# Kernel tuning notes

Hardware: AMD Instinct MI355X
Metric: run time of the kernel (lower is better)

## Reference

```python
import math
import numpy as np
import jax, jax.numpy as jnp

LMAX1, LMAX2, LMAX3 = 20, 10, 5
B_IN, RES1, RES2, RES3 = 60, 20, 10, 6
BATCH = 8


def _fact(n):
    return math.factorial(n)


def wigner_d(l, betas):
    # small Wigner-d, complex-m ordering m=-l..l; betas: [N] -> [N, 2l+1, 2l+1]
    betas = np.asarray(betas, dtype=np.float64)
    cb, sb = np.cos(betas / 2.0), np.sin(betas / 2.0)
    d = np.zeros(betas.shape + (2 * l + 1, 2 * l + 1))
    for i, mp in enumerate(range(-l, l + 1)):
        for j, m in enumerate(range(-l, l + 1)):
            pref = math.sqrt(_fact(l + mp) * _fact(l - mp) * _fact(l + m) * _fact(l - m))
            val = np.zeros_like(betas)
            for k in range(max(0, m - mp), min(l + m, l - mp) + 1):
                den = _fact(l + m - k) * _fact(k) * _fact(mp - m + k) * _fact(l - mp - k)
                val = val + ((-1.0) ** (mp - m + k)) * (pref / den) * cb ** (2 * l + m - mp - 2 * k) * sb ** (mp - m + 2 * k)
            d[..., i, j] = val
    return d


def real_U(l):
    # complex SH -> real SH change of basis
    U = np.zeros((2 * l + 1, 2 * l + 1), dtype=np.complex128)
    U[l, l] = 1.0
    for m in range(1, l + 1):
        s = (-1.0) ** m
        U[l + m, l - m] = 1.0 / math.sqrt(2.0)
        U[l + m, l + m] = s / math.sqrt(2.0)
        U[l - m, l - m] = 1j / math.sqrt(2.0)
        U[l - m, l + m] = -1j * s / math.sqrt(2.0)
    return U


def wigner_d_real(l, betas):
    U = real_U(l)
    d = wigner_d(l, betas).astype(np.complex128)
    return np.einsum('ai,nij,bj->nab', U, d, U.conj()).real


def _trig(ang, l):
    m = np.arange(-l, l + 1)
    return np.cos(np.outer(ang, m)), np.sin(np.outer(ang, m))


def flat_wigner_points(lmax, a, b, g):
    # real Wigner D on arbitrary points via D = Z(alpha) d_real(beta) Z(gamma)
    blocks = []
    for l in range(lmax + 1):
        dr = wigner_d_real(l, b)  # [N,M,M]
        cA, sA = _trig(a, l)
        cG, sG = _trig(g, l)
        T = cG[:, None, :] * dr - sG[:, None, :] * dr[:, :, ::-1]
        D = cA[:, :, None] * T + sA[:, :, None] * T[:, ::-1, :]
        blocks.append(math.sqrt(2 * l + 1) * D.reshape(len(a), -1))
    return np.concatenate(blocks, -1).astype(np.float32)


def flat_wigner_grid(lmax, alphas, betas, gammas):
    # product-grid version, flatten order (alpha, beta, gamma)
    na, nb, ng = len(alphas), len(betas), len(gammas)
    blocks = []
    for l in range(lmax + 1):
        dr = wigner_d_real(l, betas)  # [nb,M,M]
        cA, sA = _trig(alphas, l)
        cG, sG = _trig(gammas, l)
        T = cG[None, :, None, :] * dr[:, None] - sG[None, :, None, :] * dr[:, None, :, ::-1]  # [nb,ng,M,M]
        D = cA[:, None, None, :, None] * T[None] + sA[:, None, None, :, None] * T[None, :, :, ::-1, :]
        blocks.append(math.sqrt(2 * l + 1) * D.reshape(na * nb * ng, -1))
    return np.concatenate(blocks, -1).astype(np.float32)


def sph_points(lmax, a, b):
    # component-normalized real SH: Y_l(alpha,beta) = sqrt(2l+1) D^l(alpha,beta,0)[:,m=0]
    cols = []
    for l in range(lmax + 1):
        dr = wigner_d_real(l, b)[:, :, l]
        cA, sA = _trig(a, l)
        cols.append(math.sqrt(2 * l + 1) * (cA * dr + sA * dr[:, ::-1]))
    return np.concatenate(cols, -1).astype(np.float32)


def sph_grid_cols(lmax, alphas, betas):
    cols = []
    for l in range(lmax + 1):
        dr = wigner_d_real(l, betas)[:, :, l]  # [nb,M]
        cA, sA = _trig(alphas, l)
        Y = cA[None] * dr[:, None] + sA[None] * dr[:, None, ::-1]  # [nb,na,M]
        cols.append(math.sqrt(2 * l + 1) * Y)
    return np.concatenate(cols, -1)


def so3_grid(n):
    a = np.arange(n) / n * 2 * math.pi
    b = (np.arange(n) + 0.5) / n * math.pi
    g = np.arange(n) / n * 2 * math.pi
    return a, b, g


def so3_transforms(lmax_in, lmax_out, n):
    a, b, g = so3_grid(n)
    D_in = flat_wigner_grid(lmax_in, a, b, g)
    D_out = flat_wigner_grid(lmax_out, a, b, g)
    qw = np.tile(np.sin(b)[None, :, None], (n, 1, n)).ravel() * math.pi / (2.0 * n ** 3)
    return jnp.asarray(D_in), jnp.asarray((qw[:, None] * D_out).astype(np.float32))


def s2_near_identity_grid(max_beta=math.pi / 8, n_alpha=8, n_beta=3):
    beta = np.arange(1, n_beta + 1) * max_beta / n_beta
    alpha = np.linspace(0, 2 * math.pi, n_alpha + 1)[:-1]
    A, B = np.meshgrid(alpha, beta, indexing='ij')
    return A.ravel(), B.ravel()


def so3_near_identity_grid(max_beta=math.pi / 8, max_gamma=2 * math.pi, n_alpha=8, n_beta=3, n_gamma=8):
    beta = np.arange(1, n_beta + 1) * max_beta / n_beta
    alpha = np.linspace(0, 2 * math.pi, n_alpha)[:-1]
    pre_gamma = np.linspace(-max_gamma, max_gamma, n_gamma)
    A, B, preC = np.meshgrid(alpha, beta, pre_gamma, indexing='ij')
    return A.ravel(), B.ravel(), (preC - A).ravel()


# ---- constant buffers (built once with numpy, like e3nn register_buffer) ----
_betas = (np.arange(B_IN) + 0.5) / B_IN * math.pi
_alphas = np.arange(B_IN) / B_IN * 2 * math.pi
_Y = sph_grid_cols(LMAX1, _alphas, _betas)  # [nb,na,441]
_qw = np.sin(_betas) * math.pi / (2.0 * B_IN * B_IN)
FROM_S2 = jnp.asarray((_Y * _qw[:, None, None]).reshape(B_IN * B_IN, -1).astype(np.float32))  # [3600,441]

_a2, _b2 = s2_near_identity_grid()
Y_K = jnp.asarray(sph_points(LMAX1, _a2, _b2))  # [24,441]
_a3, _b3, _g3 = so3_near_identity_grid()
D_K2 = jnp.asarray(flat_wigner_points(LMAX2, _a3, _b3, _g3))  # [168,1771]
D_K3 = jnp.asarray(flat_wigner_points(LMAX3, _a3, _b3, _g3))  # [168,286]

D1_IN, D1_BWD = so3_transforms(LMAX1, LMAX2, RES1)  # [8000,12341], [8000,1771]
D2_IN, D2_BWD = so3_transforms(LMAX2, LMAX3, RES2)  # [1000,1771],  [1000,286]
D3_IN, D3_BWD = so3_transforms(LMAX3, 0, RES3)      # [216,286],    [216,1]


def _s2_linear(x, psi, lmax):
    # x [B,f_in,(lmax+1)^2] (mult-1 per l) -> so3 irreps [B,f_out,sum(2l+1)^2]
    B, fi = x.shape[0], x.shape[1]
    outs = []
    for l in range(lmax + 1):
        s, e = l * l, (l + 1) * (l + 1)
        ol = jnp.einsum('bim,iou->boum', x[:, :, s:e], psi[:, :, s:e]) / math.sqrt(fi)
        outs.append(ol.reshape(B, ol.shape[1], -1))
    return jnp.concatenate(outs, axis=-1)


def _so3_linear(x, psi, lmax):
    # block per-l linear: mult (2l+1) -> mult (2l+1)
    B, fi = x.shape[0], x.shape[1]
    outs, off = [], 0
    for l in range(lmax + 1):
        d = 2 * l + 1
        xl = x[:, :, off:off + d * d].reshape(B, fi, d, d)
        pl = psi[:, :, off:off + d * d].reshape(fi, -1, d, d)
        ol = jnp.einsum('bium,iouv->bovm', xl, pl) / math.sqrt(fi * d)
        outs.append(ol.reshape(B, ol.shape[1], -1))
        off += d * d
    return jnp.concatenate(outs, axis=-1)


def _so3_act(x, D_in, D_bwd):
    # SO3Activation: to SO(3) grid, relu, back to (lower) band-limited coeffs
    f = jax.nn.relu(jnp.einsum('bfi,ni->bfn', x, D_in))
    return jnp.einsum('bfn,ni->bfi', f, D_bwd)


def _forward(x, conv1_w, conv2_w, conv3_w, fc_w1, fc_b1, fc_w2, fc_b2):
    B = x.shape[0]
    xg = jnp.swapaxes(x, -1, -2).reshape(B, -1)  # (beta, alpha) grid, flattened
    coeff = (xg @ FROM_S2)[:, None, :]           # FromS2Grid -> [B,1,441]
    psi1 = jnp.einsum('ni,xyn->xyi', Y_K, conv1_w) / math.sqrt(Y_K.shape[0])
    h = _s2_linear(coeff, psi1, LMAX1)           # [B,64,12341]
    h = _so3_act(h, D1_IN, D1_BWD)               # [B,64,1771]
    psi2 = jnp.einsum('ni,xyn->xyi', D_K2, conv2_w) / math.sqrt(D_K2.shape[0])
    h = _so3_linear(h, psi2, LMAX2)              # [B,128,1771]
    h = _so3_act(h, D2_IN, D2_BWD)               # [B,128,286]
    psi3 = jnp.einsum('ni,xyn->xyi', D_K3, conv3_w) / math.sqrt(D_K3.shape[0])
    h = _so3_linear(h, psi3, LMAX3)              # [B,256,286]
    h = _so3_act(h, D3_IN, D3_BWD)[:, :, 0]      # lmax_out=0 -> [B,256]
    h = jax.nn.relu(h @ fc_w1 + fc_b1)           # dropout is identity in eval
    return h @ fc_w2 + fc_b2


def setup_inputs() -> dict:
    key = jax.random.key(0)
    ks = jax.random.split(key, 6)
    return {
        'x': jax.random.normal(ks[0], (BATCH, B_IN, B_IN), dtype=jnp.float32),
        'conv1_w': jax.random.normal(ks[1], (1, 64, 24), dtype=jnp.float32),
        'conv2_w': jax.random.normal(ks[2], (64, 128, 168), dtype=jnp.float32),
        'conv3_w': jax.random.normal(ks[3], (128, 256, 168), dtype=jnp.float32),
        'fc_w1': jax.random.normal(ks[4], (256, 128), dtype=jnp.float32) / math.sqrt(256.0),
        'fc_b1': jnp.zeros((128,), jnp.float32),
        'fc_w2': jax.random.normal(ks[5], (128, 10), dtype=jnp.float32) / math.sqrt(128.0),
        'fc_b2': jnp.zeros((10,), jnp.float32),
    }


def reference(x, conv1_w, conv2_w, conv3_w, fc_w1, fc_b1, fc_w2, fc_b2):
    return _forward(x, conv1_w, conv2_w, conv3_w, fc_w1, fc_b1, fc_w2, fc_b2)
```

## Files before the change

### kernel.cpp

```cpp
#include <hip/hip_runtime.h>

#define PI_D 3.14159265358979323846

constexpr int S_L20 = 12341;
constexpr int S_L10 = 1771;
constexpr int S_L5  = 286;
constexpr int C_L20 = 441;

typedef float f4 __attribute__((ext_vector_type(4)));
typedef float f2 __attribute__((ext_vector_type(2)));
template<int W> struct VW;
template<> struct VW<4> { using T = f4; };
template<> struct VW<2> { using T = f2; };

__host__ __device__ __forceinline__ int loff(int l) { return l*(4*l*l-1)/3; }

__device__ __forceinline__ int isqrt_dev(int c) {
  int l = (int)sqrtf((float)c);
  while ((l+1)*(l+1) <= c) ++l;
  while (l*l > c) --l;
  return l;
}

__device__ double d_small(int l, int mp, int m, const double* cpw, const double* spw, const double* fact) {
// ... 48 lines not shown
                                                float* t3c, float* t3s,
                                                unsigned* lut10, unsigned* lut5) {
  __shared__ double cpw[44], spw[44], fact[44];
  int b = blockIdx.x;
  int tid = threadIdx.x;
  if (b < 846) {
    float* out; int lmax, S, mode, gridn, p, chunk;
    if (b < 260)      { out=dr20g1; lmax=20; S=S_L20; mode=0; gridn=20; p=b/13;        chunk=b%13; }
    else if (b < 596) { int i=b-260; out=drK2;   lmax=10; S=S_L10; mode=1; gridn=0;  p=i/2; chunk=i%2; }
    else if (b < 636) { int i=b-596; out=dr10g1; lmax=10; S=S_L10; mode=0; gridn=20; p=i/2; chunk=i%2; }
    else if (b < 656) { int i=b-636; out=dr10g2; lmax=10; S=S_L10; mode=0; gridn=10; p=i/2; chunk=i%2; }
    else if (b < 824) { int i=b-656; out=drK3;   lmax=5;  S=S_L5;  mode=1; gridn=0;  p=i;   chunk=0; }
    else if (b < 834) { int i=b-824; out=dr5g2;  lmax=5;  S=S_L5;  mode=0; gridn=10; p=i;   chunk=0; }
    else if (b < 840) { int i=b-834; out=dr5g3;  lmax=5;  S=S_L5;  mode=0; gridn=6;  p=i;   chunk=0; }
    else              { int i=b-840; out=dr0g3;  lmax=0;  S=1;     mode=0; gridn=6;  p=i;   chunk=0; }
    double beta_ = beta_of(mode, p, gridn);
    if (tid == 0) {
      double cb_ = cos(beta_*0.5), sb_ = sin(beta_*0.5);
      cpw[0]=1.0; spw[0]=1.0; fact[0]=1.0;
      for (int i_=1;i_<44;++i_){cpw[i_]=cpw[i_-1]*cb_; spw[i_]=spw[i_-1]*sb_; fact[i_]=fact[i_-1]*(double)i_;}
    }
    __syncthreads();
    int base = chunk*1024;
    int end = min(S, base + 1024);
    for (int t = base + tid; t < end; t += 256) {
      int l = 0; while (l < lmax && t >= loff(l+1)) ++l;
      int j = t - loff(l), d = 2*l+1;
      int a = j/d, bb = j%d;
      double v = dr_elem(l, a-l, bb-l, cpw, spw, fact) * sqrt(2.0*l+1.0);
      out[(size_t)p*S + t] = (float)v;
    }
  } else if (b < 930) {
    int bb = b - 846;
    float* out; int mode, gridn, p;
    if (bb < 60) { out = drc60; mode = 0; gridn = 60; p = bb; }
    else         { out = drc24; mode = 2; gridn = 0;  p = bb - 60; }
    double beta_ = beta_of(mode, p, gridn);
    if (tid == 0) {
      double cb_ = cos(beta_*0.5), sb_ = sin(beta_*0.5);
      cpw[0]=1.0; spw[0]=1.0; fact[0]=1.0;
      for (int i_=1;i_<44;++i_){cpw[i_]=cpw[i_-1]*cb_; spw[i_]=spw[i_-1]*sb_; fact[i_]=fact[i_-1]*(double)i_;}
    }
    __syncthreads();
    for (int t = tid; t < C_L20; t += 256) {
      int l = isqrt_dev(t);
      int u = t - l*l - l;
      double v;
      if (u < 0) v = 0.0;
      else if (u == 0) v = d_small(l,0,0,cpw,spw,fact);
      else {
        double sp = (u&1)? -1.0: 1.0;
        v = 0.70710678118654752440*(d_small(l,-u,0,cpw,spw,fact) + sp*d_small(l,u,0,cpw,spw,fact));
      }
      out[(size_t)p*C_L20 + t] = (float)(v * sqrt(2.0*l+1.0));
    }
  } else if (b < 933) {
    int t = (b - 930)*256 + tid;
    if (t < 420) {
      int k = t/20, ig = t%20;
      double ang = (double)k*(double)ig*(2.0*PI_D/20.0);
      t1c[t] = (float)cos(ang); t1s[t] = (float)sin(ang);
    } else if (t < 530) {
      int i = t-420, k = i/10, ig = i%10;
      double ang = (double)k*(double)ig*(2.0*PI_D/10.0);
      t2c[i] = (float)cos(ang); t2s[i] = (float)sin(ang);
    } else if (t < 566) {
      int i = t-530, k = i/6, ig = i%6;
      double ang = (double)k*(double)ig*(2.0*PI_D/6.0);
      t3c[i] = (float)cos(ang); t3s[i] = (float)sin(ang);
    }
  } else {
    int t = (b - 933)*256 + tid;
    unsigned* lut; int s, lmax;
    if (t < S_L10) { lut = lut10; s = t; lmax = 10; }
    else if (t < S_L10 + S_L5) { lut = lut5; s = t - S_L10; lmax = 5; }
    else return;
    int l = 0; while (l < lmax && s >= loff(l+1)) ++l;
    int j = s - loff(l), d = 2*l+1;
    int u = j/d, v = j - u*d;
    lut[s] = (unsigned)l | ((unsigned)u<<8) | ((unsigned)v<<16);
  }
}

__global__ __launch_bounds__(256) void k_tab2(const float* __restrict__ drc60, float* __restrict__ FS2T,
                                              const float* __restrict__ drc24, const float* __restrict__ w1,
                                              float* __restrict__ psi1,
                                              const float* __restrict__ drk2, float* __restrict__ DK2,
                                              const float* __restrict__ drk3, float* __restrict__ DK3) {
  int b = blockIdx.x, tid = threadIdx.x;
  if (b < 6202) {
    int e = b*256 + tid;
    if (e >= 441*3600) return;
    int c = e / 3600, k = e % 3600;
    int ia = k / 60, ib = k % 60;
    int l = isqrt_dev(c);
    int u = c - l*l - l;
    double alpha = (double)ia*(2.0*PI_D/60.0);
    double beta  = ((double)ib + 0.5)*(PI_D/60.0);
    double drp = (double)drc60[ib*441 + c];
    double drn = (double)drc60[ib*441 + (c - 2*u)];
    double val = cos((double)u*alpha)*drp + sin((double)u*alpha)*drn;
    FS2T[e] = (float)(val * (sin(beta)*PI_D/(2.0*60.0*60.0)));
  } else if (b < 6313) {
    int e = (b - 6202)*256 + tid;
    if (e >= 64*441) return;
    int o = e / 441, c = e % 441;
    int l = isqrt_dev(c);
    int u = c - l*l - l;
    float acc = 0.f;
    for (int p = 0; p < 24; ++p) {
      double alpha = (double)(p/3)*(PI_D/4.0);
      double y = cos((double)u*alpha)*(double)drc24[p*441+c] + sin((double)u*alpha)*(double)drc24[p*441 + (c-2*u)];
      acc += (float)y * w1[o*24 + p];
    }
    psi1[e] = acc * 0.20412414523193150818f;
  } else {
    int e0 = (b - 6313)*256 + tid;
    const float* drk; float* DK; int S, NP, lmax, e;
    if (e0 < 168*1772) { drk = drk2; DK = DK2; S = S_L10; NP = 1772; lmax = 10; e = e0; }
    else { e = e0 - 168*1772; if (e >= 168*288) return; drk = drk3; DK = DK3; S = S_L5; NP = 288; lmax = 5; }
    int n = e / NP, idx = e % NP;
    if (idx >= S) { DK[e] = 0.f; return; }
    int l = 0; while (l < lmax && idx >= loff(l+1)) ++l;
    int j = idx - loff(l), d = 2*l+1;
    int iu = j/d, im = j%d;
    int u = iu - l, m = im - l;
    int i3 = n/24, k3 = n%8;
    double alpha = (double)i3*(2.0*PI_D/7.0);
    double gamma = (-2.0*PI_D + (double)k3*(4.0*PI_D/7.0)) - alpha;
    const float* drb = drk + (size_t)n*S + loff(l);
    double d_um   = drb[iu*d+im];
    double d_umn  = drb[iu*d + (d-1-im)];
    double d_unm  = drb[(d-1-iu)*d + im];
    double d_unmn = drb[(d-1-iu)*d + (d-1-im)];
    double cA = cos((double)u*alpha), sA = sin((double)u*alpha);
    double cG = cos((double)m*gamma), sG = sin((double)m*gamma);
    DK[e] = (float)(cA*(cG*d_um - sG*d_umn) + sA*(cG*d_unm - sG*d_unmn));
  }
}

__device__ __forceinline__ void gemm_body(const float* __restrict__ A, const float* __restrict__ B,
                                          const unsigned* __restrict__ lut, float* __restrict__ C,
                                          int M, int N, int NP, int K, int FO, int tm, int tn, float alpha,
                                          float (*As)[16][68], float (*Bs)[16][68], int tid) {
  int ty = tid/16, tx = tid%16;
  int arr = tid>>2, akq = (tid&3)*4;
  int bkk = tid>>4, bcq = (tid&15)*4;
  const float* Arow = A + (size_t)(tm + arr)*K;
  const f4 FZ = 0.f;
  float acc[4][4] = {};
  f4 ra, rb;
#define LOADC(k0)                                                        \
  if ((k0) + 16 <= K) {                                                  \
    ra = *(const f4*)&Arow[(k0) + akq];                                  \
    rb = *(const f4*)&B[(size_t)((k0) + bkk)*NP + tn + bcq];             \
  } else {                                                               \
    _Pragma("unroll")                                                    \
    for (int jj = 0; jj < 4; ++jj) {                                     \
      int k = (k0) + akq + jj;                                           \
      ra[jj] = (k < K) ? Arow[k] : 0.f;                                  \
    }                                                                    \
    int k2 = (k0) + bkk;                                                 \
    rb = (k2 < K) ? *(const f4*)&B[(size_t)k2*NP + tn + bcq] : FZ;       \
  }
#define STOREC(b)                                                        \
  {                                                                      \
    _Pragma("unroll")                                                    \
    for (int jj = 0; jj < 4; ++jj) As[b][akq+jj][arr] = ra[jj];          \
    *(f4*)&Bs[b][bkk][bcq] = rb;                                         \
  }
  LOADC(0);
  STOREC(0);
  __syncthreads();
  int cur = 0;
  for (int k0 = 0; k0 < K; k0 += 16) {
    bool nxt = (k0 + 16) < K;
    if (nxt) { LOADC(k0 + 16); }
#pragma unroll
    for (int kk = 0; kk < 16; ++kk) {
      f4 av = *(const f4*)&As[cur][kk][ty*4];
      f4 bv = *(const f4*)&Bs[cur][kk][tx*4];
#pragma unroll
      for (int q = 0; q < 4; ++q)
#pragma unroll
        for (int r2 = 0; r2 < 4; ++r2) acc[q][r2] += av[q]*bv[r2];
    }
    if (nxt) { STOREC(cur ^ 1); __syncthreads(); cur ^= 1; }
  }
#undef LOADC
#undef STOREC
  for (int q = 0; q < 4; ++q) {
    int r = tm + ty*4 + q; if (r >= M) continue;
    int i = r / FO, o = r - i*FO;
    for (int r2 = 0; r2 < 4; ++r2) {
      int c = tn + tx*4 + r2; if (c >= N) continue;
      unsigned e = lut[c];
      int l = e & 255, u = (e>>8)&255, v = (e>>16)&255;
      int d = 2*l+1;
      C[(size_t)M*loff(l) + (size_t)(i*d+u)*(FO*d) + o*d + v] = alpha*acc[q][r2];
    }
  }
}

__global__ __launch_bounds__(256) void k_gemmc(const float* __restrict__ A1, const float* __restrict__ B1,
                                               const unsigned* __restrict__ lut1, float* __restrict__ C1,
                                               int M1, int N1, int NP1, int FO1,
                                               const float* __restrict__ A2, const float* __restrict__ B2,
                                               const unsigned* __restrict__ lut2, float* __restrict__ C2,
                                               int M2, int N2, int NP2, int FO2,
                                               int K, int nbx1, int nb1, int nbx2, int nb12, float alpha,
                                               const float* __restrict__ x, const float* __restrict__ fs2T,
                                               float* __restrict__ coeff) {
  __shared__ __align__(16) float As[2][16][68], Bs[2][16][68];
  int bid = blockIdx.x, tid = threadIdx.x;
  if (bid < nb1) {
    int tm = (bid % nbx1)*64, tn = (bid / nbx1)*64;
    gemm_body(A1, B1, lut1, C1, M1, N1, NP1, K, FO1, tm, tn, alpha, As, Bs, tid);
  } else if (bid < nb12) {
    bid -= nb1;
    int tm = (bid % nbx2)*64, tn = (bid / nbx2)*64;
    gemm_body(A2, B2, lut2, C2, M2, N2, NP2, K, FO2, tm, tn, alpha, As, Bs, tid);
  } else {
    int c = bid - nb12;
    float acc[8] = {};
    const float* fr = fs2T + (size_t)c*3600;
    for (int k = tid; k < 3600; k += 256) {
      float w = fr[k];
#pragma unroll
      for (int b = 0; b < 8; ++b) acc[b] += w * x[b*3600 + k];
    }
    float* red = (float*)As;
#pragma unroll
    for (int b = 0; b < 8; ++b) red[b*256 + tid] = acc[b];
    __syncthreads();
    for (int s = 128; s > 0; s >>= 1) {
      if (tid < s) {
#pragma unroll
        for (int b = 0; b < 8; ++b) red[b*256 + tid] += red[b*256 + tid + s];
      }
      __syncthreads();
    }
    if (tid < 8) coeff[tid*441 + c] = red[tid*256];
  }
}

__global__ __launch_bounds__(256) void k_anapack(const float* __restrict__ part, const unsigned* __restrict__ lut,
                                                 float* __restrict__ hA, int FI, int S, int nch) {
  int e = blockIdx.x*256 + threadIdx.x;
  int total = 8*FI*S;
  if (e >= total) return;
  int bi = e / S, s = e - bi*S;
  float a = 0.f;
  for (int c = 0; c < nch; ++c) a += part[(size_t)c*total + e];
  unsigned u3 = lut[s];
  int l = u3 & 255, u = (u3>>8)&255, m = (u3>>16)&255;
  int d = 2*l+1;
  int b = bi / FI, i = bi - b*FI;
  hA[(size_t)8*FI*loff(l) + (size_t)(b*d+m)*(FI*d) + i*d + u] = a;
}

__global__ __launch_bounds__(256) void k_linsk(const float* __restrict__ hA, const float* __restrict__ psiP,
                                               float* __restrict__ part, int FI, int FO, int S,
                                               int maxNT, int KC) {
  int l = blockIdx.z;
  int d = 2*l+1, off = loff(l);
  int Ml = 8*d, Nl = FO*d, Kl = FI*d;
  int tm = blockIdx.x*64;
  int tn = ((int)blockIdx.y % maxNT)*64;
  int kci = (int)blockIdx.y / maxNT;
  int k0s = kci*KC;
  if (tm >= Ml || tn >= Nl || k0s >= Kl) return;
  int k1s = min(Kl, k0s + KC);
  float alpha = 1.0f/sqrtf((float)(FI*d));
  const float* Ab = hA + (size_t)8*FI*off;
  const float* Bb = psiP + (size_t)FI*FO*off;
  __shared__ __align__(16) float As[2][16][68], Bs[2][16][68];
  int tid = threadIdx.x, ty = tid/16, tx = tid%16;
  int arr = tid>>2, akq = (tid&3)*4;
  int bkk = tid>>4, bcq = (tid&15)*4;
  bool aok = (tm + arr) < Ml;
  const float* Arow = Ab + (size_t)(tm + arr)*Kl;
  const f4 FZ = 0.f;
  float acc[4][4] = {};
  f4 ra, rb;
#define LOADL(k0)                                                        \
  {                                                                      \
    ra = aok ? *(const f4*)&Arow[(k0) + akq] : FZ;                       \
    rb = *(const f4*)&Bb[(size_t)((k0) + bkk)*Nl + tn + bcq];            \
  }
#define STOREL(b)                                                        \
  {                                                                      \
    _Pragma("unroll")                                                    \
    for (int jj = 0; jj < 4; ++jj) As[b][akq+jj][arr] = ra[jj];          \
    *(f4*)&Bs[b][bkk][bcq] = rb;                                         \
  }
  LOADL(k0s);
  STOREL(0);
  __syncthreads();
  int cur = 0;
  for (int k0 = k0s; k0 < k1s; k0 += 16) {
    bool nxt = (k0 + 16) < k1s;
    if (nxt) { LOADL(k0 + 16); }
#pragma unroll
    for (int kk = 0; kk < 16; ++kk) {
      f4 av = *(const f4*)&As[cur][kk][ty*4];
      f4 bv = *(const f4*)&Bs[cur][kk][tx*4];
#pragma unroll
      for (int q = 0; q < 4; ++q)
#pragma unroll
        for (int r2 = 0; r2 < 4; ++r2) acc[q][r2] += av[q]*bv[r2];
    }
    if (nxt) { STOREL(cur ^ 1); __syncthreads(); cur ^= 1; }
  }
#undef LOADL
#undef STOREL
  size_t pbase = (size_t)kci * (size_t)8*FO*S;
  for (int q = 0; q < 4; ++q) {
    int r = tm + ty*4 + q; if (r >= Ml) continue;
    int b = r / d, m = r - b*d;
    for (int r2 = 0; r2 < 4; ++r2) {
      int c = tn + tx*4 + r2; if (c >= Nl) continue;
      int o = c / d, v = c - o*d;
      part[pbase + (size_t)(b*FO + o)*S + off + v*d + m] = alpha*acc[q][r2];
    }
  }
}

template<int L, int NG, int F, int BS>
__global__ __launch_bounds__(BS) void k_syn1b(const float* __restrict__ psi1, const float* __restrict__ coeff,
                                              const float* __restrict__ drg,
                                              const float* __restrict__ gtck, const float* __restrict__ gtsk,
                                              float* __restrict__ fw) {
  constexpr int LH = L+1;
  constexpr int LH2 = LH*LH;
  constexpr int S = (L+1)*(2*L+1)*(2*L+3)/3;
  constexpr int IGB = 4;
  constexpr int NGB = NG / IGB;
  __shared__ float PF[4*LH2], Q1F[4*LH2], Q2F[4*LH2], Q3F[4*LH2];
  __shared__ __align__(16) float uni[4*C_L20];
  __shared__ __align__(16) float tck[LH*NG], tsk[LH*NG];
  float* psi_s  = uni;
  float* coef_s = uni + 2*C_L20;
  float* Rc = uni;
  float* Rs = uni + LH*NG;
  int ib = blockIdx.x, f0 = blockIdx.y*2, b0 = blockIdx.z*2;
  int tid = threadIdx.x;
  for (int t = tid; t < C_L20; t += BS) {
    psi_s[t]          = psi1[f0*C_L20 + t];
    psi_s[C_L20 + t]  = psi1[(f0+1)*C_L20 + t];
    coef_s[t]         = coeff[b0*C_L20 + t];
    coef_s[C_L20 + t] = coeff[(b0+1)*C_L20 + t];
  }
  for (int t = tid; t < LH*NG; t += BS) { tck[t] = gtck[t]; tsk[t] = gtsk[t]; }
  __syncthreads();
  const float* drb = drg + (size_t)ib*S;
  for (int t = tid; t < LH2; t += BS) {
    int i = t / LH, j = t % LH;
    int lmin = max(i, j);
    float P[4] = {}, Q1[4] = {}, Q2[4] = {}, Q3[4] = {};
    int d = 2*lmin+1;
    int j2 = 2*j;
    int drip = loff(lmin) + (lmin+i)*d + (lmin-j);
    int drim = loff(lmin) + (lmin-i)*d + (lmin-j);
    int hA = lmin*lmin + lmin + i;
    int hB = lmin*lmin + lmin - i;
    int hM = lmin*lmin + lmin - j;
    int hMp = lmin*lmin + lmin + j;
    for (int l = lmin; l <= L; ++l) {
      float ap_ = drb[drip], app = drb[drip + j2];
      float am_ = 0.f, amp = 0.f;
      if (i > 0) { am_ = drb[drim]; amp = drb[drim + j2]; }
      float eP[2], oP[2], eM[2], oM[2];
#pragma unroll
      for (int cb = 0; cb < 2; ++cb) {
        float hm = coef_s[cb*C_L20 + hM], hmn = coef_s[cb*C_L20 + hMp];
        eP[cb] = ap_*hm + app*hmn;  oP[cb] = app*hm - ap_*hmn;
        eM[cb] = am_*hm + amp*hmn;  oM[cb] = amp*hm - am_*hmn;
      }
#pragma unroll
      for (int cf = 0; cf < 2; ++cf) {
        float ha = psi_s[cf*C_L20 + hA], hb = psi_s[cf*C_L20 + hB];
#pragma unroll
        for (int cb = 0; cb < 2; ++cb) {
          int cs = cb*2 + cf;
          P[cs]  += ha*eP[cb] + hb*eM[cb];
          Q1[cs] += ha*oP[cb] + hb*oM[cb];
          Q2[cs] += hb*eP[cb] - ha*eM[cb];
          Q3[cs] += hb*oP[cb] - ha*oM[cb];
        }
      }
      drip += d*d + d + 2*(l+i) + 3;
      drim += d*d + d + 2*(l-i) + 3;
      int hstep = d + 1;
      hA += hstep; hB += hstep; hM += hstep; hMp += hstep;
      d += 2;
    }
    if (j == 0) {
#pragma unroll
      for (int cs = 0; cs < 4; ++cs) { P[cs] *= 0.5f; Q2[cs] *= 0.5f; }
    }
#pragma unroll
    for (int cs = 0; cs < 4; ++cs) {
      PF[cs*LH2 + t] = P[cs]; Q1F[cs*LH2 + t] = Q1[cs];
      Q2F[cs*LH2 + t] = Q2[cs]; Q3F[cs*LH2 + t] = Q3[cs];
    }
  }
  __syncthreads();
  double beta = ((double)ib + 0.5) * (PI_D / (double)NG);
  float qwv = (float)(sin(beta) * PI_D / (2.0*(double)NG*(double)NG*(double)NG));
  for (int cs = 0; cs < 4; ++cs) {
    int cf = cs & 1, cb = cs >> 1;
    for (int t = tid; t < LH*NGB; t += BS) {
      int i = t / NGB, ig0 = (t % NGB)*IGB;
      f4 rc = 0.f, rs = 0.f;
      const float* Pr  = PF  + cs*LH2 + i*LH;
      const float* Q1r = Q1F + cs*LH2 + i*LH;
      const float* Q2r = Q2F + cs*LH2 + i*LH;
      const float* Q3r = Q3F + cs*LH2 + i*LH;
      for (int k = 0; k <= L; ++k) {
        float p = Pr[k], q1 = Q1r[k], q2 = Q2r[k], q3 = Q3r[k];
        f4 c = *(const f4*)(tck + k*NG + ig0);
        f4 s = *(const f4*)(tsk + k*NG + ig0);
        rc += c*p + s*q1;
        rs += c*q2 + s*q3;
      }
      *(f4*)(Rc + i*NG + ig0) = rc;
      *(f4*)(Rs + i*NG + ig0) = rs;
    }
    __syncthreads();
    size_t obase = (((size_t)(b0+cb)*F + (f0+cf))*NG + ib)*(size_t)(NG*NG);
    for (int t = tid; t < NG*NGB; t += BS) {
      int ia = t / NGB, ig0 = (t % NGB)*IGB;
      f4 acc = 0.f;
      for (int k = 0; k <= L; ++k) {
        float ca = tck[k*NG + ia], sa = tsk[k*NG + ia];
        f4 rc = *(const f4*)(Rc + k*NG + ig0);
        f4 rs = *(const f4*)(Rs + k*NG + ig0);
        acc += ca*rc - sa*rs;
      }
      f4 res;
#pragma unroll
      for (int jj = 0; jj < 4; ++jj) res[jj] = fmaxf(acc[jj], 0.0f) * qwv;
      *(f4*)(fw + obase + ia*NG + ig0) = res;
    }
    __syncthreads();
  }
}

template<int L, int NG, int F, int BS>
__global__ __launch_bounds__(BS) void k_syn(const float* __restrict__ part, int thr1, int thr2, int total,
                                            const float* __restrict__ drg,
                                            const float* __restrict__ gtck, const float* __restrict__ gtsk,
                                            float* __restrict__ fw) {
  constexpr int LH = L+1;
  constexpr int LH2 = LH*LH;
  constexpr int S = (L+1)*(2*L+1)*(2*L+3)/3;
  constexpr int RCSZ = LH*NG;
  constexpr int UNI = (S > 2*RCSZ) ? S : 2*RCSZ;
  constexpr int IGB = (NG % 4 == 0) ? 4 : 2;
  constexpr int NGB = NG / IGB;
  using VecT = typename VW<IGB>::T;
  __shared__ float PF[LH2], Q1F[LH2], Q2F[LH2], Q3F[LH2];
  __shared__ __align__(16) float uni[UNI];
  __shared__ __align__(16) float tck[LH*NG], tsk[LH*NG];
  float* hrow = uni;
  float* Rc = uni;
  float* Rs = uni + RCSZ;
  int ib = blockIdx.x, f = blockIdx.y, b = blockIdx.z;
  int tid = threadIdx.x;
  for (int t = tid; t < S; t += BS) {
    size_t e = ((size_t)b*F + f)*S + t;
    float a = part[e];
    if (t >= thr1) a += part[(size_t)total + e];
    if (t >= thr2) a += part[2*(size_t)total + e];
    hrow[t] = a;
  }
  for (int t = tid; t < LH*NG; t += BS) { tck[t] = gtck[t]; tsk[t] = gtsk[t]; }
  __syncthreads();
  const float* drb = drg + (size_t)ib*S;
  for (int t = tid; t < LH2; t += BS) {
    int i = t / LH, j = t % LH;
    int lmin = max(i, j);
    float P = 0.f, Q1 = 0.f, Q2 = 0.f, Q3 = 0.f;
    int d = 2*lmin+1;
    int j2 = 2*j;
    int drip = loff(lmin) + (lmin+i)*d + (lmin-j);
    int drim = loff(lmin) + (lmin-i)*d + (lmin-j);
    for (int l = lmin; l <= L; ++l) {
      float ap_ = drb[drip], app = drb[drip + j2];
      float am_ = 0.f, amp = 0.f;
      if (i > 0) { am_ = drb[drim]; amp = drb[drim + j2]; }
      float hp1 = hrow[drip], hp2 = hrow[drip + j2];
      float hm1 = hrow[drim], hm2 = hrow[drim + j2];
      P  += ap_*hp1 + app*hp2 + am_*hm1 + amp*hm2;
      Q1 += app*hp1 - ap_*hp2 + amp*hm1 - am_*hm2;
      Q2 += ap_*hm1 + app*hm2 - am_*hp1 - amp*hp2;
      Q3 += app*hm1 - ap_*hm2 - amp*hp1 + am_*hp2;
      drip += d*d + d + 2*(l+i) + 3;
      drim += d*d + d + 2*(l-i) + 3;
      d += 2;
    }
    if (j == 0) { P *= 0.5f; Q2 *= 0.5f; }
    PF[t] = P; Q1F[t] = Q1; Q2F[t] = Q2; Q3F[t] = Q3;
  }
  __syncthreads();
  for (int t = tid; t < LH*NGB; t += BS) {
    int i = t / NGB, ig0 = (t % NGB)*IGB;
    VecT rc = 0.f, rs = 0.f;
    const float* Pr  = PF  + i*LH;
    const float* Q1r = Q1F + i*LH;
    const float* Q2r = Q2F + i*LH;
    const float* Q3r = Q3F + i*LH;
    for (int k = 0; k <= L; ++k) {
      float p = Pr[k], q1 = Q1r[k], q2 = Q2r[k], q3 = Q3r[k];
      VecT c = *(const VecT*)(tck + k*NG + ig0);
      VecT s = *(const VecT*)(tsk + k*NG + ig0);
      rc += c*p + s*q1;
      rs += c*q2 + s*q3;
    }
    *(VecT*)(Rc + i*NG + ig0) = rc;
    *(VecT*)(Rs + i*NG + ig0) = rs;
  }
  __syncthreads();
  double beta = ((double)ib + 0.5) * (PI_D / (double)NG);
  float qwv = (float)(sin(beta) * PI_D / (2.0*(double)NG*(double)NG*(double)NG));
  size_t obase = (((size_t)b*F + f)*NG + ib)*(size_t)(NG*NG);
  for (int t = tid; t < NG*NGB; t += BS) {
    int ia = t / NGB, ig0 = (t % NGB)*IGB;
    VecT acc = 0.f;
    for (int k = 0; k <= L; ++k) {
      float ca = tck[k*NG + ia], sa = tsk[k*NG + ia];
      VecT rc = *(const VecT*)(Rc + k*NG + ig0);
// ... 81 lines not shown
        float tcv = tc[km*NG + jg];
        gcc += tcv*FcFe[k*(NH+1) + jg];
        gsc += tcv*FsFe[k*(NH+1) + jg];
      }
      for (int jg = 1; jg < NH; ++jg) {
        float tsv = ts[km*NG + jg];
        gcs += tsv*FcFo[k*(NH-1) + jg - 1];
        gss += tsv*FsFo[k*(NH-1) + jg - 1];
      }
      Gcc[k*LHP + km] = gcc; Gcs[k*LHP + km] = gcs;
      Gsc[k*LHP + km] = gsc; Gss[k*LHP + km] = gss;
    }
    __syncthreads();
#pragma unroll
    for (int e = 0; e < ME; ++e) {
      int t = tid + e*BS;
      if (t < SO) {
        unsigned u3 = lut[t];
        int l = u3 & 255, iu = (u3>>8)&255, im = (u3>>16)&255;
        int d = 2*l+1;
        int bidx = loff(l) + iu*d + im;
        int ru = (d-1-2*iu)*d, rm = d-1-2*im;
        int du_ = iu - l, dm_ = im - l;
        int ku = (du_ < 0) ? -du_ : du_;
        int km = (dm_ < 0) ? -dm_ : dm_;
        int gi = ku*LHP + km;
        float d1 = drs[bidx], d2 = drs[bidx+rm], d3 = drs[bidx+ru], d4 = drs[bidx+ru+rm];
        float g1 = Gcc[gi], g2 = Gcs[gi], g3 = Gsc[gi], g4 = Gss[gi];
        if (dm_ < 0) { g2 = -g2; g4 = -g4; }
        if (du_ < 0) { g3 = -g3; g4 = -g4; }
        rf[e] += g1*d1 - g2*d2 + g3*d3 - g4*d4;
      }
    }
    __syncthreads();
  }
  size_t obase = (size_t)ibc*((size_t)8*F*SO) + ((size_t)b*F + f)*SO;
#pragma unroll
  for (int e = 0; e < ME; ++e) {
    int t = tid + e*BS;
    if (t < SO) hpart[obase + t] = rf[e];
  }
}

__global__ __launch_bounds__(1024) void k_fc(const float* __restrict__ h4, const float* __restrict__ w1,
                                             const float* __restrict__ b1, const float* __restrict__ w2,
                                             const float* __restrict__ b2, float* __restrict__ out) {
  __shared__ float t1[1024];
  int tid = threadIdx.x;
  {
    int b = tid >> 7, j = tid & 127;
    float a = b1[j];
    const float* hr = h4 + b*256;
    for (int k = 0; k < 256; ++k) a += hr[k]*w1[k*128 + j];
    t1[tid] = fmaxf(a, 0.f);
  }
  __syncthreads();
  if (tid < 80) {
    int b = tid / 10, j = tid % 10;
    float a = b2[j];
    for (int k = 0; k < 128; ++k) a += t1[b*128 + k]*w2[k*10 + j];
    out[b*10 + j] = a;
  }
}

extern "C" void kernel_launch(void* const* d_in, const int* in_sizes, int n_in,
                              void* d_out, int out_size, void* d_ws, size_t ws_size,
                              hipStream_t stream) {
  const float* x    = (const float*)d_in[0];
  const float* w1   = (const float*)d_in[1];
  const float* w2   = (const float*)d_in[2];
  const float* w3   = (const float*)d_in[3];
  const float* fcw1 = (const float*)d_in[4];
  const float* fcb1 = (const float*)d_in[5];
  const float* fcw2 = (const float*)d_in[6];
  const float* fcb2 = (const float*)d_in[7];
  float* out = (float*)d_out;

  float* base = (float*)d_ws;
  size_t off = 0;
  auto alloc = [&](size_t n) -> float* { float* p = base + off; off += (n + 63) & ~(size_t)63; return p; };

  float* drc60  = alloc((size_t)60*441);
  float* drc24  = alloc((size_t)24*441);
  float* fs2T   = alloc((size_t)441*3600);
  float* psi1   = alloc((size_t)64*441);
  float* coeff  = alloc((size_t)8*441);
  float* drK2   = alloc((size_t)168*S_L10);
  float* drK3   = alloc((size_t)168*S_L5);
  float* dk2    = alloc((size_t)168*1772 + 64);
  float* dk3    = alloc((size_t)168*288 + 64);
  float* psi2P  = alloc((size_t)8192*S_L10);
  float* psi3P  = alloc((size_t)32768*S_L5);
  float* dr20g1 = alloc((size_t)20*S_L20);
  float* dr10g1 = alloc((size_t)20*S_L10);
  float* dr10g2 = alloc((size_t)10*S_L10);
  float* dr5g2  = alloc((size_t)10*S_L5);
  float* dr5g3  = alloc((size_t)6*S_L5);
  float* dr0g3  = alloc(6);
  float* t1ck   = alloc((size_t)21*20);
  float* t1sk   = alloc((size_t)21*20);
  float* t2ck   = alloc((size_t)11*10);
  float* t2sk   = alloc((size_t)11*10);
  float* t3ck   = alloc((size_t)6*6);
  float* t3sk   = alloc((size_t)6*6);
  float* lut10  = alloc((size_t)S_L10);
  float* lut5   = alloc((size_t)S_L5);
  float* fwbuf  = alloc((size_t)8*64*8000);
  float* scr    = alloc((size_t)3*8*128*S_L10);
  float* hA2    = alloc((size_t)8*64*S_L10);
  float* hA3    = alloc((size_t)8*128*S_L5);
  float* h4     = alloc((size_t)8*256);
  if (off * sizeof(float) > ws_size) return;

  const float inv_s168 = 0.07715167498104595f;
  const int KC = 512;

  k_tables<<<dim3(942), 256, 0, stream>>>(dr20g1, drK2, dr10g1, dr10g2, drK3, dr5g2, dr5g3, dr0g3,
                                          drc60, drc24, t1ck, t1sk, t2ck, t2sk, t3ck, t3sk,
                                          (unsigned*)lut10, (unsigned*)lut5);
  k_tab2<<<dim3(7665), 256, 0, stream>>>(drc60, fs2T, drc24, w1, psi1, drK2, dk2, drK3, dk3);
  k_gemmc<<<dim3(3584 + 2560 + 441), 256, 0, stream>>>(
      w2, dk2, (const unsigned*)lut10, psi2P, 8192,  S_L10, 1772, 128,
      w3, dk3, (const unsigned*)lut5,  psi3P, 32768, S_L5,  288,  256,
      168, 128, 3584, 512, 6144, inv_s168, x, fs2T, coeff);

  k_syn1b<20,20,64,256><<<dim3(20,32,4), 256, 0, stream>>>(psi1, coeff, dr20g1, t1ck, t1sk, fwbuf);
  k_ana<10,20,64,4,256><<<dim3(64,8,5),  256, 0, stream>>>(fwbuf, dr10g1, t1ck, t1sk, scr);
  k_anapack<<<dim3((8*64*S_L10+255)/256), 256, 0, stream>>>(scr, (const unsigned*)lut10, hA2, 64, S_L10, 5);
  k_linsk<<<dim3(3, 42*3, 11), 256, 0, stream>>>(hA2, psi2P, scr, 64, 128, S_L10, 42, KC);
  k_syn<10,10,128,128><<<dim3(10,128,8), 128, 0, stream>>>(scr, 84, 680, 8*128*S_L10, dr10g2, t2ck, t2sk, fwbuf);
  k_ana<5,10,128,5,128><<<dim3(128,8,2),  128, 0, stream>>>(fwbuf, dr5g2, t2ck, t2sk, scr);
  k_anapack<<<dim3((8*128*S_L5+255)/256), 256, 0, stream>>>(scr, (const unsigned*)lut5, hA3, 128, S_L5, 2);
  k_linsk<<<dim3(2, 44*3, 6), 256, 0, stream>>>(hA3, psi3P, scr, 128, 256, S_L5, 44, KC);
  k_syn<5,6,256,64><<<dim3(6,256,8), 64, 0, stream>>>(scr, 10, 84, 8*256*S_L5, dr5g3, t3ck, t3sk, fwbuf);
  k_ana<0,6,256,6,64><<<dim3(256,8,1), 64, 0, stream>>>(fwbuf, dr0g3, t3ck, t3sk, h4);
  k_fc<<<dim3(1), 1024, 0, stream>>>(h4, fcw1, fcb1, fcw2, fcb2, out);
}
```

Measured before the change: 635.2 us.

## Fuse S2 quadrature into coefficient reduction and merge syn1b into GEMM launch

The precomputed 441x3600 S2 Fourier table is removed. The input-to-coefficient projection is now computed directly in k_tab2, with per-block cos/sin tables held in shared memory, so the large table is neither written nor read back. The first synthesis stage (syn1b) moves into the same launch as the psi2/psi3 GEMMs, which removes one kernel launch and lets the two workloads run side by side. This raises the shared-memory footprint of the combined kernel, which may reduce GEMM occupancy.

```diff
diff --git a/kernel.cpp b/kernel.cpp
--- a/kernel.cpp
+++ b/kernel.cpp
@@ -154,27 +154,17 @@
   }
 }
 
-__global__ __launch_bounds__(256) void k_tab2(const float* __restrict__ drc60, float* __restrict__ FS2T,
-                                              const float* __restrict__ drc24, const float* __restrict__ w1,
+__global__ __launch_bounds__(256) void k_tab2(const float* __restrict__ drc24, const float* __restrict__ w1,
                                               float* __restrict__ psi1,
                                               const float* __restrict__ drk2, float* __restrict__ DK2,
-                                              const float* __restrict__ drk3, float* __restrict__ DK3) {
+                                              const float* __restrict__ drk3, float* __restrict__ DK3,
+                                              const float* __restrict__ drc60, const float* __restrict__ x,
+                                              float* __restrict__ coeff) {
+  __shared__ float red[2048];
+  __shared__ float cu[60], su[60], sbq[60];
   int b = blockIdx.x, tid = threadIdx.x;
-  if (b < 6202) {
+  if (b < 111) {
     int e = b*256 + tid;
-    if (e >= 441*3600) return;
-    int c = e / 3600, k = e % 3600;
-    int ia = k / 60, ib = k % 60;
-    int l = isqrt_dev(c);
-    int u = c - l*l - l;
-    double alpha = (double)ia*(2.0*PI_D/60.0);
-    double beta  = ((double)ib + 0.5)*(PI_D/60.0);
-    double drp = (double)drc60[ib*441 + c];
-    double drn = (double)drc60[ib*441 + (c - 2*u)];
-    double val = cos((double)u*alpha)*drp + sin((double)u*alpha)*drn;
-    FS2T[e] = (float)(val * (sin(beta)*PI_D/(2.0*60.0*60.0)));
-  } else if (b < 6313) {
-    int e = (b - 6202)*256 + tid;
     if (e >= 64*441) return;
     int o = e / 441, c = e % 441;
     int l = isqrt_dev(c);
@@ -186,8 +176,8 @@
       acc += (float)y * w1[o*24 + p];
     }
     psi1[e] = acc * 0.20412414523193150818f;
-  } else {
-    int e0 = (b - 6313)*256 + tid;
+  } else if (b < 1463) {
+    int e0 = (b - 111)*256 + tid;
     const float* drk; float* DK; int S, NP, lmax, e;
     if (e0 < 168*1772) { drk = drk2; DK = DK2; S = S_L10; NP = 1772; lmax = 10; e = e0; }
     else { e = e0 - 168*1772; if (e >= 168*288) return; drk = drk3; DK = DK3; S = S_L5; NP = 288; lmax = 5; }
@@ -208,6 +198,38 @@
     double cA = cos((double)u*alpha), sA = sin((double)u*alpha);
     double cG = cos((double)m*gamma), sG = sin((double)m*gamma);
     DK[e] = (float)(cA*(cG*d_um - sG*d_umn) + sA*(cG*d_unm - sG*d_unmn));
+  } else {
+    int c = b - 1463;
+    int l = isqrt_dev(c);
+    int u = c - l*l - l;
+    int cneg = c - 2*u;
+    if (tid < 60) {
+      double alpha = (double)tid*(2.0*PI_D/60.0);
+      double beta  = ((double)tid + 0.5)*(PI_D/60.0);
+      cu[tid]  = (float)cos((double)u*alpha);
+      su[tid]  = (float)sin((double)u*alpha);
+      sbq[tid] = (float)(sin(beta)*PI_D/(2.0*60.0*60.0));
+    }
+    __syncthreads();
+    float acc[8] = {};
+    for (int k = tid; k < 3600; k += 256) {
+      int ia = k / 60, ib2 = k % 60;
+      double val = (double)cu[ia]*(double)drc60[ib2*441 + c] + (double)su[ia]*(double)drc60[ib2*441 + cneg];
+      float w = (float)(val) * sbq[ib2];
+#pragma unroll
+      for (int bb = 0; bb < 8; ++bb) acc[bb] += w * x[bb*3600 + k];
+    }
+#pragma unroll
+    for (int bb = 0; bb < 8; ++bb) red[bb*256 + tid] = acc[bb];
+    __syncthreads();
+    for (int s = 128; s > 0; s >>= 1) {
+      if (tid < s) {
+#pragma unroll
+        for (int bb = 0; bb < 8; ++bb) red[bb*256 + tid] += red[bb*256 + tid + s];
+      }
+      __syncthreads();
+    }
+    if (tid < 8) coeff[tid*441 + c] = red[tid*256];
   }
 }
 
@@ -274,45 +296,155 @@
   }
 }
 
-__global__ __launch_bounds__(256) void k_gemmc(const float* __restrict__ A1, const float* __restrict__ B1,
-                                               const unsigned* __restrict__ lut1, float* __restrict__ C1,
-                                               int M1, int N1, int NP1, int FO1,
-                                               const float* __restrict__ A2, const float* __restrict__ B2,
-                                               const unsigned* __restrict__ lut2, float* __restrict__ C2,
-                                               int M2, int N2, int NP2, int FO2,
-                                               int K, int nbx1, int nb1, int nbx2, int nb12, float alpha,
-                                               const float* __restrict__ x, const float* __restrict__ fs2T,
-                                               float* __restrict__ coeff) {
-  __shared__ __align__(16) float As[2][16][68], Bs[2][16][68];
+__device__ void syn1b_body(const float* __restrict__ psi1, const float* __restrict__ coeff,
+                           const float* __restrict__ drg,
+                           const float* __restrict__ gtck, const float* __restrict__ gtsk,
+                           float* __restrict__ fw, int ib, int f0, int b0, int tid,
+                           float* PF, float* Q1F, float* Q2F, float* Q3F,
+                           float* uni, float* tck, float* tsk) {
+  constexpr int L = 20, NG = 20, F = 64, BS = 256;
+  constexpr int LH = L+1;
+  constexpr int LH2 = LH*LH;
+  constexpr int S = S_L20;
+  constexpr int IGB = 4;
+  constexpr int NGB = NG / IGB;
+  float* psi_s  = uni;
+  float* coef_s = uni + 2*C_L20;
+  float* Rc = uni;
+  float* Rs = uni + LH*NG;
+  for (int t = tid; t < C_L20; t += BS) {
+    psi_s[t]          = psi1[f0*C_L20 + t];
+    psi_s[C_L20 + t]  = psi1[(f0+1)*C_L20 + t];
+    coef_s[t]         = coeff[b0*C_L20 + t];
+    coef_s[C_L20 + t] = coeff[(b0+1)*C_L20 + t];
+  }
+  for (int t = tid; t < LH*NG; t += BS) { tck[t] = gtck[t]; tsk[t] = gtsk[t]; }
+  __syncthreads();
+  const float* drb = drg + (size_t)ib*S;
+  for (int t = tid; t < LH2; t += BS) {
+    int i = t / LH, j = t % LH;
+    int lmin = max(i, j);
+    float P[4] = {}, Q1[4] = {}, Q2[4] = {}, Q3[4] = {};
+    int d = 2*lmin+1;
+    int j2 = 2*j;
+    int drip = loff(lmin) + (lmin+i)*d + (lmin-j);
+    int drim = loff(lmin) + (lmin-i)*d + (lmin-j);
+    int hA = lmin*lmin + lmin + i;
+    int hB = lmin*lmin + lmin - i;
+    int hM = lmin*lmin + lmin - j;
+    int hMp = lmin*lmin + lmin + j;
+    for (int l = lmin; l <= L; ++l) {
+      float ap_ = drb[drip], app = drb[drip + j2];
+      float am_ = 0.f, amp = 0.f;
+      if (i > 0) { am_ = drb[drim]; amp = drb[drim + j2]; }
+      float eP[2], oP[2], eM[2], oM[2];
+#pragma unroll
+      for (int cb = 0; cb < 2; ++cb) {
+        float hm = coef_s[cb*C_L20 + hM], hmn = coef_s[cb*C_L20 + hMp];
+        eP[cb] = ap_*hm + app*hmn;  oP[cb] = app*hm - ap_*hmn;
+        eM[cb] = am_*hm + amp*hmn;  oM[cb] = amp*hm - am_*hmn;
+      }
+#pragma unroll
+      for (int cf = 0; cf < 2; ++cf) {
+        float ha = psi_s[cf*C_L20 + hA], hb = psi_s[cf*C_L20 + hB];
+#pragma unroll
+        for (int cb = 0; cb < 2; ++cb) {
+          int cs = cb*2 + cf;
+          P[cs]  += ha*eP[cb] + hb*eM[cb];
+          Q1[cs] += ha*oP[cb] + hb*oM[cb];
+          Q2[cs] += hb*eP[cb] - ha*eM[cb];
+          Q3[cs] += hb*oP[cb] - ha*oM[cb];
+        }
+      }
+      drip += d*d + d + 2*(l+i) + 3;
+      drim += d*d + d + 2*(l-i) + 3;
+      int hstep = d + 1;
+      hA += hstep; hB += hstep; hM += hstep; hMp += hstep;
+      d += 2;
+    }
+    if (j == 0) {
+#pragma unroll
+      for (int cs = 0; cs < 4; ++cs) { P[cs] *= 0.5f; Q2[cs] *= 0.5f; }
+    }
+#pragma unroll
+    for (int cs = 0; cs < 4; ++cs) {
+      PF[cs*LH2 + t] = P[cs]; Q1F[cs*LH2 + t] = Q1[cs];
+      Q2F[cs*LH2 + t] = Q2[cs]; Q3F[cs*LH2 + t] = Q3[cs];
+    }
+  }
+  __syncthreads();
+  double beta = ((double)ib + 0.5) * (PI_D / (double)NG);
+  float qwv = (float)(sin(beta) * PI_D / (2.0*(double)NG*(double)NG*(double)NG));
+  for (int cs = 0; cs < 4; ++cs) {
+    int cf = cs & 1, cb = cs >> 1;
+    for (int t = tid; t < LH*NGB; t += BS) {
+      int i = t / NGB, ig0 = (t % NGB)*IGB;
+      f4 rc = 0.f, rs = 0.f;
+      const float* Pr  = PF  + cs*LH2 + i*LH;
+      const float* Q1r = Q1F + cs*LH2 + i*LH;
+      const float* Q2r = Q2F + cs*LH2 + i*LH;
+      const float* Q3r = Q3F + cs*LH2 + i*LH;
+      for (int k = 0; k <= L; ++k) {
+        float p = Pr[k], q1 = Q1r[k], q2 = Q2r[k], q3 = Q3r[k];
+        f4 c = *(const f4*)(tck + k*NG + ig0);
+        f4 s = *(const f4*)(tsk + k*NG + ig0);
+        rc += c*p + s*q1;
+        rs += c*q2 + s*q3;
+      }
+      *(f4*)(Rc + i*NG + ig0) = rc;
+      *(f4*)(Rs + i*NG + ig0) = rs;
+    }
+    __syncthreads();
+    size_t obase = (((size_t)(b0+cb)*F + (f0+cf))*NG + ib)*(size_t)(NG*NG);
+    for (int t = tid; t < NG*NGB; t += BS) {
+      int ia = t / NGB, ig0 = (t % NGB)*IGB;
+      f4 acc = 0.f;
+      for (int k = 0; k <= L; ++k) {
+        float ca = tck[k*NG + ia], sa = tsk[k*NG + ia];
+        f4 rc = *(const f4*)(Rc + k*NG + ig0);
+        f4 rs = *(const f4*)(Rs + k*NG + ig0);
+        acc += ca*rc - sa*rs;
+      }
+      f4 res;
+#pragma unroll
+      for (int jj = 0; jj < 4; ++jj) res[jj] = fmaxf(acc[jj], 0.0f) * qwv;
+      *(f4*)(fw + obase + ia*NG + ig0) = res;
+    }
+    __syncthreads();
+  }
+}
+
+__global__ __launch_bounds__(256) void k_gs(const float* __restrict__ A1, const float* __restrict__ B1,
+                                            const unsigned* __restrict__ lut1, float* __restrict__ C1,
+                                            int M1, int N1, int NP1, int FO1,
+                                            const float* __restrict__ A2, const float* __restrict__ B2,
+                                            const unsigned* __restrict__ lut2, float* __restrict__ C2,
+                                            int M2, int N2, int NP2, int FO2,
+                                            int K, int nbx1, int nb1, int nbx2, int nb12, float alpha,
+                                            const float* __restrict__ psi1, const float* __restrict__ coeff,
+                                            const float* __restrict__ dr20g1,
+                                            const float* __restrict__ t1ck, const float* __restrict__ t1sk,
+                                            float* __restrict__ fwbuf) {
+  __shared__ __align__(16) float shbuf[9664];
   int bid = blockIdx.x, tid = threadIdx.x;
   if (bid < nb1) {
     int tm = (bid % nbx1)*64, tn = (bid / nbx1)*64;
-    gemm_body(A1, B1, lut1, C1, M1, N1, NP1, K, FO1, tm, tn, alpha, As, Bs, tid);
+    gemm_body(A1, B1, lut1, C1, M1, N1, NP1, K, FO1, tm, tn, alpha,
+              (float(*)[16][68])shbuf, (float(*)[16][68])(shbuf + 2176), tid);
   } else if (bid < nb12) {
-    bid -= nb1;
-    int tm = (bid % nbx2)*64, tn = (bid / nbx2)*64;
-    gemm_body(A2, B2, lut2, C2, M2, N2, NP2, K, FO2, tm, tn, alpha, As, Bs, tid);
+    int b2 = bid - nb1;
+    int tm = (b2 % nbx2)*64, tn = (b2 / nbx2)*64;
+    gemm_body(A2, B2, lut2, C2, M2, N2, NP2, K, FO2, tm, tn, alpha,
+              (float(*)[16][68])shbuf, (float(*)[16][68])(shbuf + 2176), tid);
   } else {
-    int c = bid - nb12;
-    float acc[8] = {};
-    const float* fr = fs2T + (size_t)c*3600;
-    for (int k = tid; k < 3600; k += 256) {
-      float w = fr[k];
-#pragma unroll
-      for (int b = 0; b < 8; ++b) acc[b] += w * x[b*3600 + k];
-    }
-    float* red = (float*)As;
-#pragma unroll
-    for (int b = 0; b < 8; ++b) red[b*256 + tid] = acc[b];
-    __syncthreads();
-    for (int s = 128; s > 0; s >>= 1) {
-      if (tid < s) {
-#pragma unroll
-        for (int b = 0; b < 8; ++b) red[b*256 + tid] += red[b*256 + tid + s];
-      }
-      __syncthreads();
-    }
-    if (tid < 8) coeff[tid*441 + c] = red[tid*256];
+    int b2 = bid - nb12;
+    int ib = b2 % 20;
+    int r = b2 / 20;
+    int f0 = (r % 32)*2;
+    int b0 = (r / 32)*2;
+    syn1b_body(psi1, coeff, dr20g1, t1ck, t1sk, fwbuf, ib, f0, b0, tid,
+               shbuf, shbuf + 1764, shbuf + 3528, shbuf + 5292,
+               shbuf + 7056, shbuf + 8820, shbuf + 9240);
   }
 }
 
@@ -399,127 +531,6 @@
 }
 
 template<int L, int NG, int F, int BS>
-__global__ __launch_bounds__(BS) void k_syn1b(const float* __restrict__ psi1, const float* __restrict__ coeff,
-                                              const float* __restrict__ drg,
-                                              const float* __restrict__ gtck, const float* __restrict__ gtsk,
-                                              float* __restrict__ fw) {
-  constexpr int LH = L+1;
-  constexpr int LH2 = LH*LH;
-  constexpr int S = (L+1)*(2*L+1)*(2*L+3)/3;
-  constexpr int IGB = 4;
-  constexpr int NGB = NG / IGB;
-  __shared__ float PF[4*LH2], Q1F[4*LH2], Q2F[4*LH2], Q3F[4*LH2];
-  __shared__ __align__(16) float uni[4*C_L20];
-  __shared__ __align__(16) float tck[LH*NG], tsk[LH*NG];
-  float* psi_s  = uni;
-  float* coef_s = uni + 2*C_L20;
-  float* Rc = uni;
-  float* Rs = uni + LH*NG;
-  int ib = blockIdx.x, f0 = blockIdx.y*2, b0 = blockIdx.z*2;
-  int tid = threadIdx.x;
-  for (int t = tid; t < C_L20; t += BS) {
-    psi_s[t]          = psi1[f0*C_L20 + t];
-    psi_s[C_L20 + t]  = psi1[(f0+1)*C_L20 + t];
-    coef_s[t]         = coeff[b0*C_L20 + t];
-    coef_s[C_L20 + t] = coeff[(b0+1)*C_L20 + t];
-  }
-  for (int t = tid; t < LH*NG; t += BS) { tck[t] = gtck[t]; tsk[t] = gtsk[t]; }
-  __syncthreads();
-  const float* drb = drg + (size_t)ib*S;
-  for (int t = tid; t < LH2; t += BS) {
-    int i = t / LH, j = t % LH;
-    int lmin = max(i, j);
-    float P[4] = {}, Q1[4] = {}, Q2[4] = {}, Q3[4] = {};
-    int d = 2*lmin+1;
-    int j2 = 2*j;
-    int drip = loff(lmin) + (lmin+i)*d + (lmin-j);
-    int drim = loff(lmin) + (lmin-i)*d + (lmin-j);
-    int hA = lmin*lmin + lmin + i;
-    int hB = lmin*lmin + lmin - i;
-    int hM = lmin*lmin + lmin - j;
-    int hMp = lmin*lmin + lmin + j;
-    for (int l = lmin; l <= L; ++l) {
-      float ap_ = drb[drip], app = drb[drip + j2];
-      float am_ = 0.f, amp = 0.f;
-      if (i > 0) { am_ = drb[drim]; amp = drb[drim + j2]; }
-      float eP[2], oP[2], eM[2], oM[2];
-#pragma unroll
-      for (int cb = 0; cb < 2; ++cb) {
-        float hm = coef_s[cb*C_L20 + hM], hmn = coef_s[cb*C_L20 + hMp];
-        eP[cb] = ap_*hm + app*hmn;  oP[cb] = app*hm - ap_*hmn;
-        eM[cb] = am_*hm + amp*hmn;  oM[cb] = amp*hm - am_*hmn;
-      }
-#pragma unroll
-      for (int cf = 0; cf < 2; ++cf) {
-        float ha = psi_s[cf*C_L20 + hA], hb = psi_s[cf*C_L20 + hB];
-#pragma unroll
-        for (int cb = 0; cb < 2; ++cb) {
-          int cs = cb*2 + cf;
-          P[cs]  += ha*eP[cb] + hb*eM[cb];
-          Q1[cs] += ha*oP[cb] + hb*oM[cb];
-          Q2[cs] += hb*eP[cb] - ha*eM[cb];
-          Q3[cs] += hb*oP[cb] - ha*oM[cb];
-        }
-      }
-      drip += d*d + d + 2*(l+i) + 3;
-      drim += d*d + d + 2*(l-i) + 3;
-      int hstep = d + 1;
-      hA += hstep; hB += hstep; hM += hstep; hMp += hstep;
-      d += 2;
-    }
-    if (j == 0) {
-#pragma unroll
-      for (int cs = 0; cs < 4; ++cs) { P[cs] *= 0.5f; Q2[cs] *= 0.5f; }
-    }
-#pragma unroll
-    for (int cs = 0; cs < 4; ++cs) {
-      PF[cs*LH2 + t] = P[cs]; Q1F[cs*LH2 + t] = Q1[cs];
-      Q2F[cs*LH2 + t] = Q2[cs]; Q3F[cs*LH2 + t] = Q3[cs];
-    }
-  }
-  __syncthreads();
-  double beta = ((double)ib + 0.5) * (PI_D / (double)NG);
-  float qwv = (float)(sin(beta) * PI_D / (2.0*(double)NG*(double)NG*(double)NG));
-  for (int cs = 0; cs < 4; ++cs) {
-    int cf = cs & 1, cb = cs >> 1;
-    for (int t = tid; t < LH*NGB; t += BS) {
-      int i = t / NGB, ig0 = (t % NGB)*IGB;
-      f4 rc = 0.f, rs = 0.f;
-      const float* Pr  = PF  + cs*LH2 + i*LH;
-      const float* Q1r = Q1F + cs*LH2 + i*LH;
-      const float* Q2r = Q2F + cs*LH2 + i*LH;
-      const float* Q3r = Q3F + cs*LH2 + i*LH;
-      for (int k = 0; k <= L; ++k) {
-        float p = Pr[k], q1 = Q1r[k], q2 = Q2r[k], q3 = Q3r[k];
-        f4 c = *(const f4*)(tck + k*NG + ig0);
-        f4 s = *(const f4*)(tsk + k*NG + ig0);
-        rc += c*p + s*q1;
-        rs += c*q2 + s*q3;
-      }
-      *(f4*)(Rc + i*NG + ig0) = rc;
-      *(f4*)(Rs + i*NG + ig0) = rs;
-    }
-    __syncthreads();
-    size_t obase = (((size_t)(b0+cb)*F + (f0+cf))*NG + ib)*(size_t)(NG*NG);
-    for (int t = tid; t < NG*NGB; t += BS) {
-      int ia = t / NGB, ig0 = (t % NGB)*IGB;
-      f4 acc = 0.f;
-      for (int k = 0; k <= L; ++k) {
-        float ca = tck[k*NG + ia], sa = tsk[k*NG + ia];
-        f4 rc = *(const f4*)(Rc + k*NG + ig0);
-        f4 rs = *(const f4*)(Rs + k*NG + ig0);
-        acc += ca*rc - sa*rs;
-      }
-      f4 res;
-#pragma unroll
-      for (int jj = 0; jj < 4; ++jj) res[jj] = fmaxf(acc[jj], 0.0f) * qwv;
-      *(f4*)(fw + obase + ia*NG + ig0) = res;
-    }
-    __syncthreads();
-  }
-}
-
-template<int L, int NG, int F, int BS>
 __global__ __launch_bounds__(BS) void k_syn(const float* __restrict__ part, int thr1, int thr2, int total,
                                             const float* __restrict__ drg,
                                             const float* __restrict__ gtck, const float* __restrict__ gtsk,
@@ -767,7 +778,6 @@
 
   float* drc60  = alloc((size_t)60*441);
   float* drc24  = alloc((size_t)24*441);
-  float* fs2T   = alloc((size_t)441*3600);
   float* psi1   = alloc((size_t)64*441);
   float* coeff  = alloc((size_t)8*441);
   float* drK2   = alloc((size_t)168*S_L10);
@@ -803,13 +813,13 @@
   k_tables<<<dim3(942), 256, 0, stream>>>(dr20g1, drK2, dr10g1, dr10g2, drK3, dr5g2, dr5g3, dr0g3,
                                           drc60, drc24, t1ck, t1sk, t2ck, t2sk, t3ck, t3sk,
                                           (unsigned*)lut10, (unsigned*)lut5);
-  k_tab2<<<dim3(7665), 256, 0, stream>>>(drc60, fs2T, drc24, w1, psi1, drK2, dk2, drK3, dk3);
-  k_gemmc<<<dim3(3584 + 2560 + 441), 256, 0, stream>>>(
+  k_tab2<<<dim3(1904), 256, 0, stream>>>(drc24, w1, psi1, drK2, dk2, drK3, dk3, drc60, x, coeff);
+  k_gs<<<dim3(3584 + 2560 + 2560), 256, 0, stream>>>(
       w2, dk2, (const unsigned*)lut10, psi2P, 8192,  S_L10, 1772, 128,
       w3, dk3, (const unsigned*)lut5,  psi3P, 32768, S_L5,  288,  256,
-      168, 128, 3584, 512, 6144, inv_s168, x, fs2T, coeff);
-
-  k_syn1b<20,20,64,256><<<dim3(20,32,4), 256, 0, stream>>>(psi1, coeff, dr20g1, t1ck, t1sk, fwbuf);
+      168, 128, 3584, 512, 6144, inv_s168,
+      psi1, coeff, dr20g1, t1ck, t1sk, fwbuf);
+
   k_ana<10,20,64,4,256><<<dim3(64,8,5),  256, 0, stream>>>(fwbuf, dr10g1, t1ck, t1sk, scr);
   k_anapack<<<dim3((8*64*S_L10+255)/256), 256, 0, stream>>>(scr, (const unsigned*)lut10, hA2, 64, S_L10, 5);
   k_linsk<<<dim3(3, 42*3, 11), 256, 0, stream>>>(hA2, psi2P, scr, 64, 128, S_L10, 42, KC);
```

Result: faster. 612.6 us (median of 2 runs) (-3.6%).
